# Kernel optimization log

Measured on AMD Instinct MI355X. Metric: run time of the kernel, lower is better.

## Reference

```python
import jax, jax.numpy as jnp
import numpy as np

EMB = 16
L = 100
B = 8192
BN_EPS = 1e-5


def _bn(x, g, b):
    # BatchNorm1d in training mode: biased batch stats over dim 0. x: [b, EMB]
    mu = jnp.mean(x, axis=0)
    var = jnp.mean((x - mu) ** 2, axis=0)
    return g * (x - mu) / jnp.sqrt(var + BN_EPS) + b


def _pool(me, aw, g6, b6, a6):
    # me: [b, L, EMB] masked embeddings; aw: [b, L, 1] masked attention logits
    s = jnp.sum(me, axis=1)                       # sum pool
    mean = jnp.mean(me, axis=1)                   # mean over full L (incl. padding), as in torch
    sq = me * me
    l2 = jnp.sum(sq, axis=-1)                     # [b, L]
    mx_i = jnp.argmax(l2, axis=1)                 # first max, matches torch.max
    mn_i = jnp.argmin(jnp.where(l2 == 0, jnp.asarray(9999.0, l2.dtype), l2), axis=1)
    mx = jnp.take_along_axis(me, mx_i[:, None, None], axis=1)[:, 0]
    mn = jnp.take_along_axis(me, mn_i[:, None, None], axis=1)[:, 0]
    attw = jax.nn.softmax(aw, axis=1)             # softmax over L incl. zeroed pads (faithful)
    at = jnp.sum(me * attw, axis=1)
    ko = 0.5 * (s * s - jnp.sum(sq, axis=1))      # korder (FM-style)
    ko = ko / jnp.maximum(jnp.linalg.norm(ko, axis=-1, keepdims=True), 1e-12)
    # branch order: sum, mean, max, min, korder, atten (matches torch.cat order)
    pools = jnp.stack([
        _bn(s, g6[0], b6[0]), _bn(mean, g6[1], b6[1]), _bn(mx, g6[2], b6[2]),
        _bn(mn, g6[3], b6[3]), _bn(ko, g6[4], b6[4]), _bn(at, g6[5], b6[5])], axis=1)
    w = jax.nn.softmax(a6)[None, :, None]
    return jnp.sum(pools * w, axis=1)             # [b, EMB]


def setup_inputs() -> dict:
    key = jax.random.key(0)
    ks = jax.random.split(key, 24)
    f32 = jnp.float32
    inp = {
        'uid': jax.random.randint(ks[0], (B,), 0, 139000),
        'mid': jax.random.randint(ks[1], (B,), 0, 132000),
        'yr': jax.random.randint(ks[2], (B,), 0, 150),
        'ids_ug': jax.random.randint(ks[3], (B, L), 0, 30),
        'ids_urb': jax.random.randint(ks[4], (B, L), 0, 132000),
        'ids_mg': jax.random.randint(ks[5], (B, L), 0, 30),
        'ids_mt': jax.random.randint(ks[6], (B, L), 0, 41000),
        'len_ug': jax.random.randint(ks[7], (B,), 1, L + 1),
        'len_urb': jax.random.randint(ks[8], (B,), 1, L + 1),
        'len_mg': jax.random.randint(ks[9], (B,), 1, L + 1),
        'len_mt': jax.random.randint(ks[10], (B,), 1, L + 1),
        'emb_userId': jax.random.normal(ks[11], (139000, EMB), f32) * 0.05,
        'emb_movieId': jax.random.normal(ks[12], (132000, EMB), f32) * 0.05,
        'emb_tagId': jax.random.normal(ks[13], (41000, EMB), f32) * 0.05,
        'emb_genreId': jax.random.normal(ks[14], (30, EMB), f32) * 0.05,
        'emb_year': jax.random.normal(ks[15], (150, EMB), f32) * 0.05,
        # init_param(): atten embeddings ~ N(1.0, 1e-6)
        'att_movieId': 1.0 + jax.random.normal(ks[16], (132000, 1), f32) * 1e-6,
        'att_tagId': 1.0 + jax.random.normal(ks[17], (41000, 1), f32) * 1e-6,
        'att_genreId': 1.0 + jax.random.normal(ks[18], (30, 1), f32) * 1e-6,
        'bn_gamma': jnp.ones((4, 6, EMB), f32),
        'bn_beta': jnp.zeros((4, 6, EMB), f32),
        'alpha': jnp.ones((4, 6), f32),
        'W1': jax.random.normal(ks[19], (112, 64), f32) * 0.05,
        'b1': jnp.zeros((64,), f32),
        'W2': jax.random.normal(ks[20], (64, 32), f32) * 0.05,
        'b2': jnp.zeros((32,), f32),
        'W3': jax.random.normal(ks[21], (32, 1), f32) * 0.05,
        'b3': jnp.zeros((1,), f32),
    }
    return inp


def reference(uid, mid, yr, ids_ug, ids_urb, ids_mg, ids_mt,
              len_ug, len_urb, len_mg, len_mt,
              emb_userId, emb_movieId, emb_tagId, emb_genreId, emb_year,
              att_movieId, att_tagId, att_genreId,
              bn_gamma, bn_beta, alpha, W1, b1, W2, b2, W3, b3):
    emb1 = jnp.concatenate([emb_userId[uid], emb_movieId[mid], emb_year[yr]], axis=1)  # [b, 48]
    ar = jnp.arange(L)
    fields = [
        (ids_ug, len_ug, emb_genreId, att_genreId),
        (ids_urb, len_urb, emb_movieId, att_movieId),
        (ids_mg, len_mg, emb_genreId, att_genreId),
        (ids_mt, len_mt, emb_tagId, att_tagId),
    ]
    pooled = []
    for i, (ids, ln, tab, atab) in enumerate(fields):
        m = (ln[:, None] > ar)[..., None].astype(tab.dtype)  # [b, L, 1]
        me = tab[ids] * m
        aw = atab[ids] * m
        pooled.append(_pool(me, aw, bn_gamma[i], bn_beta[i], alpha[i]))
    x = jnp.concatenate([emb1] + pooled, axis=1)  # [b, 112]
    h = jax.nn.relu(x @ W1 + b1)
    h = jax.nn.relu(h @ W2 + b2)
    return jax.nn.sigmoid(h @ W3 + b3)[:, 0]
```

## Files before the change

kernel.cpp:

```cpp
#include <hip/hip_runtime.h>
#include <math.h>

#define BATCH 8192
#define L 100
#define EMB 16
#define NCH 384

#define POOLED_FLOATS (4 * BATCH * 96)
#define POOLED_BYTES  (POOLED_FLOATS * 4)

__global__ __launch_bounds__(256) void pool_kernel(
    const int* __restrict__ ids_ug, const int* __restrict__ ids_urb,
    const int* __restrict__ ids_mg, const int* __restrict__ ids_mt,
    const int* __restrict__ len_ug, const int* __restrict__ len_urb,
    const int* __restrict__ len_mg, const int* __restrict__ len_mt,
    const float* __restrict__ emb_movie, const float* __restrict__ emb_tag,
    const float* __restrict__ emb_genre,
    const float* __restrict__ att_movie, const float* __restrict__ att_tag,
    const float* __restrict__ att_genre,
    float* __restrict__ pooled, double* __restrict__ sums, double* __restrict__ sumsqs)
{
    const int f = blockIdx.y;
    const int* ids; const int* lens; const float* tab; const float* atab;
    switch (f) {
        case 0: ids = ids_ug;  lens = len_ug;  tab = emb_genre; atab = att_genre; break;
        case 1: ids = ids_urb; lens = len_urb; tab = emb_movie; atab = att_movie; break;
        case 2: ids = ids_mg;  lens = len_mg;  tab = emb_genre; atab = att_genre; break;
        default:ids = ids_mt;  lens = len_mt;  tab = emb_tag;   atab = att_tag;   break;
    }
    const int tid = threadIdx.x;
    const int sub = tid >> 4;
    const int e   = tid & 15;
    const int j   = e >> 2;
    const int c   = e & 3;
    const int b   = blockIdx.x * 16 + sub;
    const int ln  = lens[b];

    const int* idrow = ids + (size_t)b * L;
    const float4* __restrict__ tab4 = (const float4*)tab;

    __shared__ float l2buf[16][100][2];

    float4 s   = make_float4(0.f, 0.f, 0.f, 0.f);
    float4 ssq = s, att = s;
    float expsum = 0.f;

    int l = j;
    for (; l + 4 < ln; l += 8) {
        const int id0 = idrow[l];
        const int id1 = idrow[l + 4];
        const float4 v0 = tab4[(size_t)id0 * 4 + c];
        const float4 v1 = tab4[(size_t)id1 * 4 + c];
        const float aw0 = atab[id0];
        const float aw1 = atab[id1];
        float4 w0, w1;
        w0.x = v0.x * v0.x; w0.y = v0.y * v0.y; w0.z = v0.z * v0.z; w0.w = v0.w * v0.w;
        w1.x = v1.x * v1.x; w1.y = v1.y * v1.y; w1.z = v1.z * v1.z; w1.w = v1.w * v1.w;
        s.x += v0.x + v1.x; s.y += v0.y + v1.y; s.z += v0.z + v1.z; s.w += v0.w + v1.w;
        ssq.x += w0.x + w1.x; ssq.y += w0.y + w1.y;
        ssq.z += w0.z + w1.z; ssq.w += w0.w + w1.w;
        float p0 = (w0.x + w0.y) + (w0.z + w0.w);
        float p1 = (w1.x + w1.y) + (w1.z + w1.w);
        p0 += __shfl_xor(p0, 1);
        p1 += __shfl_xor(p1, 1);
        l2buf[sub][l][c >> 1]     = p0;
        l2buf[sub][l + 4][c >> 1] = p1;
        const float e0 = __expf(aw0);
        const float e1 = __expf(aw1);
        expsum += e0 + e1;
        att.x += v0.x * e0 + v1.x * e1; att.y += v0.y * e0 + v1.y * e1;
        att.z += v0.z * e0 + v1.z * e1; att.w += v0.w * e0 + v1.w * e1;
    }
    if (l < ln) {
        const int id0 = idrow[l];
        const float4 v0 = tab4[(size_t)id0 * 4 + c];
        const float aw0 = atab[id0];
        float4 w0;
        w0.x = v0.x * v0.x; w0.y = v0.y * v0.y; w0.z = v0.z * v0.z; w0.w = v0.w * v0.w;
        s.x += v0.x; s.y += v0.y; s.z += v0.z; s.w += v0.w;
        ssq.x += w0.x; ssq.y += w0.y; ssq.z += w0.z; ssq.w += w0.w;
        float p0 = (w0.x + w0.y) + (w0.z + w0.w);
        p0 += __shfl_xor(p0, 1);
        l2buf[sub][l][c >> 1] = p0;
        const float e0 = __expf(aw0);
        expsum += e0;
        att.x += v0.x * e0; att.y += v0.y * e0; att.z += v0.z * e0; att.w += v0.w * e0;
    }
    __syncthreads();

    float bmx = -1e30f; int lx = 0x7fffffff;
    float bmn =  1e30f; int lm = 0x7fffffff;
    for (int q = e; q < ln; q += 16) {
        float2 t = *(float2*)&l2buf[sub][q][0];
        float l2 = t.x + t.y;
        if (l2 > bmx) { bmx = l2; lx = q; }
        float l2m = (l2 == 0.0f) ? 9999.0f : l2;
        if (l2m < bmn) { bmn = l2m; lm = q; }
    }
    #pragma unroll
    for (int m = 1; m <= 8; m <<= 1) {
        float o  = __shfl_xor(bmx, m);
        int   ol = __shfl_xor(lx, m);
        if (o > bmx || (o == bmx && ol < lx)) { bmx = o; lx = ol; }
        float on  = __shfl_xor(bmn, m);
        int   onl = __shfl_xor(lm, m);
        if (on < bmn || (on == bmn && onl < lm)) { bmn = on; lm = onl; }
    }

    #pragma unroll
    for (int m = 4; m <= 8; m <<= 1) {
        s.x += __shfl_xor(s.x, m); s.y += __shfl_xor(s.y, m);
        s.z += __shfl_xor(s.z, m); s.w += __shfl_xor(s.w, m);
        ssq.x += __shfl_xor(ssq.x, m); ssq.y += __shfl_xor(ssq.y, m);
        ssq.z += __shfl_xor(ssq.z, m); ssq.w += __shfl_xor(ssq.w, m);
        att.x += __shfl_xor(att.x, m); att.y += __shfl_xor(att.y, m);
        att.z += __shfl_xor(att.z, m); att.w += __shfl_xor(att.w, m);
        expsum += __shfl_xor(expsum, m);
    }
    expsum += (float)(L - ln);

    float4 mean;
    mean.x = s.x * (1.0f / L); mean.y = s.y * (1.0f / L);
    mean.z = s.z * (1.0f / L); mean.w = s.w * (1.0f / L);
    float4 ko;
    ko.x = 0.5f * (s.x * s.x - ssq.x); ko.y = 0.5f * (s.y * s.y - ssq.y);
    ko.z = 0.5f * (s.z * s.z - ssq.z); ko.w = 0.5f * (s.w * s.w - ssq.w);
    float pk = (ko.x * ko.x + ko.y * ko.y) + (ko.z * ko.z + ko.w * ko.w);
    float kn2 = pk + __shfl_xor(pk, 1);
    kn2 += __shfl_xor(kn2, 2);
    float rn = 1.0f / fmaxf(sqrtf(kn2), 1e-12f);
    ko.x *= rn; ko.y *= rn; ko.z *= rn; ko.w *= rn;
    float ie = 1.0f / expsum;
    att.x *= ie; att.y *= ie; att.z *= ie; att.w *= ie;

    float4 mxv = make_float4(0.f, 0.f, 0.f, 0.f), mnv = mxv;
    if (e < 4) {
        mxv = tab4[(size_t)idrow[lx] * 4 + e];
        mnv = tab4[(size_t)idrow[lm] * 4 + e];
    }

    __syncthreads();
    float* tile = (float*)l2buf;

    if (e < 4) {
        float4 pv[6] = { s, mean, mxv, mnv, ko, att };
        float4* prow = (float4*)(pooled + ((size_t)(f * BATCH + b)) * 96);
        #pragma unroll
        for (int p = 0; p < 6; ++p) {
            prow[p * 4 + e] = pv[p];
            *(float4*)&tile[sub * 100 + p * 16 + e * 4] = pv[p];
        }
    }
    __syncthreads();
    if (tid < 96) {
        float sm = 0.f, sq = 0.f;
        #pragma unroll
        for (int s2 = 0; s2 < 16; ++s2) {
            float x = tile[s2 * 100 + tid];
            sm += x;
            sq += x * x;
        }
        atomicAdd(&sums[f * 96 + tid],   (double)sm);
        atomicAdd(&sumsqs[f * 96 + tid], (double)sq);
    }
}

__global__ __launch_bounds__(384) void coef_kernel(
    const double* __restrict__ sums, const double* __restrict__ sumsqs,
    const float* __restrict__ gamma, const float* __restrict__ beta,
    const float* __restrict__ alpha,
    float* __restrict__ coefA, float* __restrict__ coefB)
{
    int c = threadIdx.x;
    if (c >= NCH) return;
    int f = c / 96;
    int p = (c % 96) >> 4;
    double mu  = sums[c]   * (1.0 / BATCH);
    double var = sumsqs[c] * (1.0 / BATCH) - mu * mu;
    float inv = (float)(1.0 / sqrt(var + 1e-5));
    float g  = gamma[c];
    float bb = beta[c];
    float amax = -1e30f;
    for (int q = 0; q < 6; ++q) amax = fmaxf(amax, alpha[f * 6 + q]);
    float wsum = 0.f;
    for (int q = 0; q < 6; ++q) wsum += __expf(alpha[f * 6 + q] - amax);
    float wp = __expf(alpha[f * 6 + p] - amax) / wsum;
    float muf = (float)mu;
    coefA[c] = wp * g * inv;
    coefB[c] = wp * (bb - g * muf * inv);
}

#define SPB 16
__global__ __launch_bounds__(256) void final_kernel(
    const int* __restrict__ uid, const int* __restrict__ mid, const int* __restrict__ yr,
    const float* __restrict__ emb_user, const float* __restrict__ emb_movie,
    const float* __restrict__ emb_year,
    const float* __restrict__ pooled,
    const float* __restrict__ coefA, const float* __restrict__ coefB,
    const float* __restrict__ W1, const float* __restrict__ b1,
    const float* __restrict__ W2, const float* __restrict__ b2,
    const float* __restrict__ W3, const float* __restrict__ b3,
    float* __restrict__ out)
{
    __shared__ float sW1[112 * 64];
    __shared__ float sW2[64 * 32];
    __shared__ float sW3[32];
    __shared__ float sb1[64];
    __shared__ float sb2[32];
    __shared__ float xt[SPB][112];
    __shared__ float h1t[SPB][64];

    const int tid = threadIdx.x;
    for (int i = tid; i < 112 * 16; i += 256)
        ((float4*)sW1)[i] = ((const float4*)W1)[i];
    for (int i = tid; i < 64 * 8; i += 256)
        ((float4*)sW2)[i] = ((const float4*)W2)[i];
    if (tid < 32) sW3[tid] = W3[tid];
    if (tid < 64) sb1[tid] = b1[tid];
    if (tid < 32) sb2[tid] = b2[tid];

    const int sub = tid >> 4;
    const int e   = tid & 15;
    const int b   = blockIdx.x * SPB + sub;

    xt[sub][e]      = emb_user [(size_t)uid[b] * EMB + e];
    xt[sub][16 + e] = emb_movie[(size_t)mid[b] * EMB + e];
    xt[sub][32 + e] = emb_year [(size_t)yr[b]  * EMB + e];

    #pragma unroll
    for (int f = 0; f < 4; ++f) {
        const float* pr = pooled + ((size_t)(f * BATCH + b)) * 96;
        float acc = 0.f;
        #pragma unroll
        for (int p = 0; p < 6; ++p) {
            int c = f * 96 + p * 16 + e;
            acc += coefA[c] * pr[p * 16 + e] + coefB[c];
        }
        xt[sub][48 + f * 16 + e] = acc;
    }
    __syncthreads();

    float4 h1 = ((float4*)sb1)[e];
    for (int k = 0; k < 112; ++k) {
        float xk = xt[sub][k];
        float4 w = ((float4*)sW1)[k * 16 + e];
        h1.x += xk * w.x; h1.y += xk * w.y; h1.z += xk * w.z; h1.w += xk * w.w;
    }
    float4 h1r;
    h1r.x = fmaxf(h1.x, 0.f); h1r.y = fmaxf(h1.y, 0.f);
    h1r.z = fmaxf(h1.z, 0.f); h1r.w = fmaxf(h1.w, 0.f);
    *(float4*)&h1t[sub][e * 4] = h1r;
    __syncthreads();

    float2 h2 = ((float2*)sb2)[e];
    for (int k = 0; k < 64; ++k) {
        float hk = h1t[sub][k];
        float2 w = ((float2*)sW2)[k * 16 + e];
        h2.x += hk * w.x; h2.y += hk * w.y;
    }
    float part = fmaxf(h2.x, 0.f) * sW3[2 * e] + fmaxf(h2.y, 0.f) * sW3[2 * e + 1];
    part += __shfl_xor(part, 1);
    part += __shfl_xor(part, 2);
    part += __shfl_xor(part, 4);
    part += __shfl_xor(part, 8);
    if (e == 0) {
        float t = part + b3[0];
        out[b] = 1.f / (1.f + __expf(-t));
    }
}

extern "C" void kernel_launch(void* const* d_in, const int* in_sizes, int n_in,
                              void* d_out, int out_size, void* d_ws, size_t ws_size,
                              hipStream_t stream) {
    const int* uid     = (const int*)d_in[0];
    const int* mid     = (const int*)d_in[1];
    const int* yr      = (const int*)d_in[2];
    const int* ids_ug  = (const int*)d_in[3];
    const int* ids_urb = (const int*)d_in[4];
    const int* ids_mg  = (const int*)d_in[5];
    const int* ids_mt  = (const int*)d_in[6];
    const int* len_ug  = (const int*)d_in[7];
    const int* len_urb = (const int*)d_in[8];
    const int* len_mg  = (const int*)d_in[9];
    const int* len_mt  = (const int*)d_in[10];
    const float* emb_user  = (const float*)d_in[11];
    const float* emb_movie = (const float*)d_in[12];
    const float* emb_tag   = (const float*)d_in[13];
    const float* emb_genre = (const float*)d_in[14];
    const float* emb_year  = (const float*)d_in[15];
    const float* att_movie = (const float*)d_in[16];
    const float* att_tag   = (const float*)d_in[17];
    const float* att_genre = (const float*)d_in[18];
    const float* bn_gamma  = (const float*)d_in[19];
    const float* bn_beta   = (const float*)d_in[20];
    const float* alpha     = (const float*)d_in[21];
    const float* W1 = (const float*)d_in[22];
    const float* b1 = (const float*)d_in[23];
    const float* W2 = (const float*)d_in[24];
    const float* b2 = (const float*)d_in[25];
    const float* W3 = (const float*)d_in[26];
    const float* b3 = (const float*)d_in[27];
    float* out = (float*)d_out;

    float*  pooled = (float*)d_ws;
    double* sums   = (double*)((char*)d_ws + POOLED_BYTES);
    double* sumsqs = sums + NCH;
    float*  coefA  = (float*)(sums + 2 * NCH);
    float*  coefB  = coefA + NCH;

    hipMemsetAsync(sums, 0, 2 * NCH * sizeof(double), stream);
    pool_kernel<<<dim3(BATCH / 16, 4), 256, 0, stream>>>(
        ids_ug, ids_urb, ids_mg, ids_mt,
        len_ug, len_urb, len_mg, len_mt,
        emb_movie, emb_tag, emb_genre,
        att_movie, att_tag, att_genre,
        pooled, sums, sumsqs);
    coef_kernel<<<1, 384, 0, stream>>>(sums, sumsqs, bn_gamma, bn_beta, alpha,
                                       coefA, coefB);
    final_kernel<<<BATCH / SPB, 256, 0, stream>>>(
        uid, mid, yr, emb_user, emb_movie, emb_year,
        pooled, coefA, coefB, W1, b1, W2, b2, W3, b3, out);
}
```

Before: 177.1 us.

## Unroll pool gather loop 4x with masked tails and halve block size

The pooling loop now handles four sequence positions per iteration, using clamped indices and multiplicative masks in place of a separate tail branch. This puts more independent gathers in flight per thread to hide memory latency. Blocks shrink to 8 samples and 128 threads, which doubles the block count and the atomic reductions. The l2 buffer is cut to one float per position, reduced via extra shuffles and written by one lane, with padding to 113 or 112.

Result: slower. 200.9 us (+13.4%).

```diff
diff --git a/kernel.cpp b/kernel.cpp
--- a/kernel.cpp
+++ b/kernel.cpp
@@ -9,7 +9,9 @@
 #define POOLED_FLOATS (4 * BATCH * 96)
 #define POOLED_BYTES  (POOLED_FLOATS * 4)
 
-__global__ __launch_bounds__(256) void pool_kernel(
+#define SPB_POOL 8
+
+__global__ __launch_bounds__(128) void pool_kernel(
     const int* __restrict__ ids_ug, const int* __restrict__ ids_urb,
     const int* __restrict__ ids_mg, const int* __restrict__ ids_mt,
     const int* __restrict__ len_ug, const int* __restrict__ len_urb,
@@ -33,66 +35,78 @@
     const int e   = tid & 15;
     const int j   = e >> 2;
     const int c   = e & 3;
-    const int b   = blockIdx.x * 16 + sub;
+    const int b   = blockIdx.x * SPB_POOL + sub;
     const int ln  = lens[b];
+    const int lnm1 = ln - 1;
 
     const int* idrow = ids + (size_t)b * L;
     const float4* __restrict__ tab4 = (const float4*)tab;
 
-    __shared__ float l2buf[16][100][2];
+    __shared__ float l2buf[SPB_POOL][113];
 
     float4 s   = make_float4(0.f, 0.f, 0.f, 0.f);
     float4 ssq = s, att = s;
     float expsum = 0.f;
 
-    int l = j;
-    for (; l + 4 < ln; l += 8) {
-        const int id0 = idrow[l];
-        const int id1 = idrow[l + 4];
-        const float4 v0 = tab4[(size_t)id0 * 4 + c];
-        const float4 v1 = tab4[(size_t)id1 * 4 + c];
-        const float aw0 = atab[id0];
-        const float aw1 = atab[id1];
-        float4 w0, w1;
-        w0.x = v0.x * v0.x; w0.y = v0.y * v0.y; w0.z = v0.z * v0.z; w0.w = v0.w * v0.w;
-        w1.x = v1.x * v1.x; w1.y = v1.y * v1.y; w1.z = v1.z * v1.z; w1.w = v1.w * v1.w;
-        s.x += v0.x + v1.x; s.y += v0.y + v1.y; s.z += v0.z + v1.z; s.w += v0.w + v1.w;
-        ssq.x += w0.x + w1.x; ssq.y += w0.y + w1.y;
-        ssq.z += w0.z + w1.z; ssq.w += w0.w + w1.w;
-        float p0 = (w0.x + w0.y) + (w0.z + w0.w);
-        float p1 = (w1.x + w1.y) + (w1.z + w1.w);
-        p0 += __shfl_xor(p0, 1);
-        p1 += __shfl_xor(p1, 1);
-        l2buf[sub][l][c >> 1]     = p0;
-        l2buf[sub][l + 4][c >> 1] = p1;
-        const float e0 = __expf(aw0);
-        const float e1 = __expf(aw1);
-        expsum += e0 + e1;
-        att.x += v0.x * e0 + v1.x * e1; att.y += v0.y * e0 + v1.y * e1;
-        att.z += v0.z * e0 + v1.z * e1; att.w += v0.w * e0 + v1.w * e1;
-    }
-    if (l < ln) {
-        const int id0 = idrow[l];
-        const float4 v0 = tab4[(size_t)id0 * 4 + c];
-        const float aw0 = atab[id0];
-        float4 w0;
-        w0.x = v0.x * v0.x; w0.y = v0.y * v0.y; w0.z = v0.z * v0.z; w0.w = v0.w * v0.w;
-        s.x += v0.x; s.y += v0.y; s.z += v0.z; s.w += v0.w;
-        ssq.x += w0.x; ssq.y += w0.y; ssq.z += w0.z; ssq.w += w0.w;
-        float p0 = (w0.x + w0.y) + (w0.z + w0.w);
-        p0 += __shfl_xor(p0, 1);
-        l2buf[sub][l][c >> 1] = p0;
-        const float e0 = __expf(aw0);
-        expsum += e0;
-        att.x += v0.x * e0; att.y += v0.y * e0; att.z += v0.z * e0; att.w += v0.w * e0;
+    for (int l = j; l < ln; l += 16) {
+        const int l1 = l + 4, l2i = l + 8, l3 = l + 12;
+        const int ida = idrow[l];
+        const int idb = idrow[min(l1, lnm1)];
+        const int idc = idrow[min(l2i, lnm1)];
+        const int idd = idrow[min(l3, lnm1)];
+        const float4 va = tab4[(size_t)ida * 4 + c];
+        const float4 vb = tab4[(size_t)idb * 4 + c];
+        const float4 vc = tab4[(size_t)idc * 4 + c];
+        const float4 vd = tab4[(size_t)idd * 4 + c];
+        const float awa = atab[ida];
+        const float awb = atab[idb];
+        const float awc = atab[idc];
+        const float awd = atab[idd];
+        const float mb = (l1  < ln) ? 1.f : 0.f;
+        const float mc = (l2i < ln) ? 1.f : 0.f;
+        const float md = (l3  < ln) ? 1.f : 0.f;
+        float4 vbm, vcm, vdm;
+        vbm.x = vb.x * mb; vbm.y = vb.y * mb; vbm.z = vb.z * mb; vbm.w = vb.w * mb;
+        vcm.x = vc.x * mc; vcm.y = vc.y * mc; vcm.z = vc.z * mc; vcm.w = vc.w * mc;
+        vdm.x = vd.x * md; vdm.y = vd.y * md; vdm.z = vd.z * md; vdm.w = vd.w * md;
+        s.x += va.x + vbm.x + vcm.x + vdm.x;
+        s.y += va.y + vbm.y + vcm.y + vdm.y;
+        s.z += va.z + vbm.z + vcm.z + vdm.z;
+        s.w += va.w + vbm.w + vcm.w + vdm.w;
+        ssq.x += va.x * va.x + vbm.x * vb.x + vcm.x * vc.x + vdm.x * vd.x;
+        ssq.y += va.y * va.y + vbm.y * vb.y + vcm.y * vc.y + vdm.y * vd.y;
+        ssq.z += va.z * va.z + vbm.z * vb.z + vcm.z * vc.z + vdm.z * vd.z;
+        ssq.w += va.w * va.w + vbm.w * vb.w + vcm.w * vc.w + vdm.w * vd.w;
+        const float ea = __expf(awa);
+        const float eb = __expf(awb);
+        const float ec = __expf(awc);
+        const float ed = __expf(awd);
+        expsum += ea + eb * mb + ec * mc + ed * md;
+        att.x += va.x * ea + vbm.x * eb + vcm.x * ec + vdm.x * ed;
+        att.y += va.y * ea + vbm.y * eb + vcm.y * ec + vdm.y * ed;
+        att.z += va.z * ea + vbm.z * eb + vcm.z * ec + vdm.z * ed;
+        att.w += va.w * ea + vbm.w * eb + vcm.w * ec + vdm.w * ed;
+        float pa = va.x * va.x + va.y * va.y + va.z * va.z + va.w * va.w;
+        float pb = vbm.x * vb.x + vbm.y * vb.y + vbm.z * vb.z + vbm.w * vb.w;
+        float pc = vcm.x * vc.x + vcm.y * vc.y + vcm.z * vc.z + vcm.w * vc.w;
+        float pd = vdm.x * vd.x + vdm.y * vd.y + vdm.z * vd.z + vdm.w * vd.w;
+        pa += __shfl_xor(pa, 1); pa += __shfl_xor(pa, 2);
+        pb += __shfl_xor(pb, 1); pb += __shfl_xor(pb, 2);
+        pc += __shfl_xor(pc, 1); pc += __shfl_xor(pc, 2);
+        pd += __shfl_xor(pd, 1); pd += __shfl_xor(pd, 2);
+        if (c == 0) {
+            l2buf[sub][l]   = pa;
+            l2buf[sub][l1]  = pb;
+            l2buf[sub][l2i] = pc;
+            l2buf[sub][l3]  = pd;
+        }
     }
     __syncthreads();
 
     float bmx = -1e30f; int lx = 0x7fffffff;
     float bmn =  1e30f; int lm = 0x7fffffff;
     for (int q = e; q < ln; q += 16) {
-        float2 t = *(float2*)&l2buf[sub][q][0];
-        float l2 = t.x + t.y;
+        float l2 = l2buf[sub][q];
         if (l2 > bmx) { bmx = l2; lx = q; }
         float l2m = (l2 == 0.0f) ? 9999.0f : l2;
         if (l2m < bmn) { bmn = l2m; lm = q; }
@@ -148,15 +162,15 @@
         #pragma unroll
         for (int p = 0; p < 6; ++p) {
             prow[p * 4 + e] = pv[p];
-            *(float4*)&tile[sub * 100 + p * 16 + e * 4] = pv[p];
+            *(float4*)&tile[sub * 112 + p * 16 + e * 4] = pv[p];
         }
     }
     __syncthreads();
     if (tid < 96) {
         float sm = 0.f, sq = 0.f;
         #pragma unroll
-        for (int s2 = 0; s2 < 16; ++s2) {
-            float x = tile[s2 * 100 + tid];
+        for (int s2 = 0; s2 < SPB_POOL; ++s2) {
+            float x = tile[s2 * 112 + tid];
             sm += x;
             sq += x * x;
         }
@@ -309,7 +323,7 @@
     float*  coefB  = coefA + NCH;
 
     hipMemsetAsync(sums, 0, 2 * NCH * sizeof(double), stream);
-    pool_kernel<<<dim3(BATCH / 16, 4), 256, 0, stream>>>(
+    pool_kernel<<<dim3(BATCH / SPB_POOL, 4), 128, 0, stream>>>(
         ids_ug, ids_urb, ids_mg, ids_mt,
         len_ug, len_urb, len_mg, len_mt,
         emb_movie, emb_tag, emb_genre,
```
